# Kernel tuning notes

Measured on AMD Instinct MI355X. Metric: run time of the kernel, lower is better.

Reference implementation:

```python
import jax, jax.numpy as jnp
import numpy as np

EPS = 1e-6  # matches torch F.normalize eps used in pytorch3d lighting

def _normalize(x):
    n = jnp.linalg.norm(x, axis=-1, keepdims=True)
    return x / jnp.maximum(n, EPS)

def _interp(pix_to_face, bary, face_attrs):
    # interpolate_face_attributes: (N,H,W,K), (N,H,W,K,3), (F,3,D) -> (N,H,W,K,D)
    mask = (pix_to_face < 0)[..., None]
    idx = jnp.maximum(pix_to_face, 0)
    vals = face_attrs[idx]                      # (N,H,W,K,3,D) gather
    out = jnp.einsum('nhwkv,nhwkvd->nhwkd', bary, vals)
    return jnp.where(mask, 0.0, out)

def setup_inputs() -> dict:
    key = jax.random.key(0)
    ks = jax.random.split(key, 16)
    N, H, W, K = 8, 512, 512, 1
    V, F = 100000, 200000
    p2f = jax.random.randint(ks[0], (N, H, W, K), 0, F)
    bg = jax.random.uniform(ks[1], (N, H, W, K)) < 0.1
    pix_to_face = jnp.where(bg, -1, p2f)
    bary = jax.random.uniform(ks[2], (N, H, W, K, 3))
    bary = bary / bary.sum(-1, keepdims=True)             # valid barycentrics
    verts = jax.random.normal(ks[3], (V, 3), dtype=jnp.float32)
    verts_normals = _normalize(jax.random.normal(ks[4], (V, 3), dtype=jnp.float32))
    verts_colors = jax.random.uniform(ks[5], (V, 3), dtype=jnp.float32)
    faces = jax.random.randint(ks[6], (F, 3), 0, V)
    return {
        'pix_to_face': pix_to_face,
        'bary_coords': bary.astype(jnp.float32),
        'verts': verts,
        'verts_normals': verts_normals,
        'verts_colors': verts_colors,
        'faces': faces,
        'light_location': jax.random.normal(ks[7], (N, 3), dtype=jnp.float32) * 3.0,
        'light_ambient': jnp.full((1, 3), 0.5, jnp.float32),
        'light_diffuse': jnp.full((1, 3), 0.3, jnp.float32),
        'light_specular': jnp.full((1, 3), 0.2, jnp.float32),
        'mat_ambient': jnp.ones((1, 3), jnp.float32),
        'mat_diffuse': jnp.ones((1, 3), jnp.float32),
        'mat_specular': jnp.ones((1, 3), jnp.float32),
        'shininess': jnp.array([64.0], jnp.float32),
        'camera_pos': jax.random.normal(ks[8], (N, 3), dtype=jnp.float32) * 3.0,
        'background': jnp.ones((3,), jnp.float32),
    }

def reference(pix_to_face, bary_coords, verts, verts_normals, verts_colors, faces,
              light_location, light_ambient, light_diffuse, light_specular,
              mat_ambient, mat_diffuse, mat_specular, shininess,
              camera_pos, background):
    # ---- texture sampling (TexturesVertex) + face-attribute interpolation ----
    faces_verts = verts[faces]            # (F,3,3)
    faces_normals = verts_normals[faces]  # (F,3,3)
    faces_colors = verts_colors[faces]    # (F,3,3)
    points = _interp(pix_to_face, bary_coords, faces_verts)    # (N,H,W,K,3)
    normals = _interp(pix_to_face, bary_coords, faces_normals) # (N,H,W,K,3)
    texels = _interp(pix_to_face, bary_coords, faces_colors)   # (N,H,W,K,3)
    # ---- per-pixel Phong lighting (PointLights) ----
    loc = light_location[:, None, None, None, :]
    cam = camera_pos[:, None, None, None, :]
    n = _normalize(normals)
    to_light = _normalize(loc - points)
    cos_angle = (n * to_light).sum(-1)                         # (N,H,W,K)
    light_diff = light_diffuse * jnp.maximum(cos_angle, 0.0)[..., None]
    smask = (cos_angle > 0).astype(points.dtype)
    cos_m = cos_angle * smask
    view_dir = _normalize(cam - points)
    reflect = -to_light + 2.0 * cos_m[..., None] * n
    alpha = jnp.maximum((view_dir * reflect).sum(-1), 0.0) * smask
    alpha_safe = jnp.where(alpha > 0, alpha, 1.0)
    spec_pow = jnp.where(alpha > 0, alpha_safe ** shininess, 0.0)
    light_spec = light_specular * spec_pow[..., None]
    ambient = mat_ambient * light_ambient                       # (1,3)
    diffuse = mat_diffuse * light_diff
    specular = mat_specular * light_spec
    colors = (ambient + diffuse) * texels + specular            # (N,H,W,K,3)
    # ---- hard RGB blend ----
    is_bg = pix_to_face[..., 0] < 0                             # (N,H,W)
    rgb = jnp.where(is_bg[..., None], background, colors[..., 0, :])
    a = (~is_bg).astype(rgb.dtype)[..., None]
    return jnp.concatenate([rgb, a], axis=-1)                   # (N,H,W,4)
```

## Files before the change

kernel.cpp:

```cpp
#include <hip/hip_runtime.h>
#include <hip/hip_bf16.h>

#define EPS 1e-6f

__device__ __forceinline__ float3 ld3(const float* p, int i) {
    return make_float3(p[3*i+0], p[3*i+1], p[3*i+2]);
}
__device__ __forceinline__ float3 add3(float3 a, float3 b) {
    return make_float3(a.x+b.x, a.y+b.y, a.z+b.z);
}
__device__ __forceinline__ float3 sub3(float3 a, float3 b) {
    return make_float3(a.x-b.x, a.y-b.y, a.z-b.z);
}
__device__ __forceinline__ float3 scale3(float s, float3 a) {
    return make_float3(s*a.x, s*a.y, s*a.z);
}
__device__ __forceinline__ float dot3(float3 a, float3 b) {
    return a.x*b.x + a.y*b.y + a.z*b.z;
}
__device__ __forceinline__ float3 norm3(float3 a) {
    float n = sqrtf(dot3(a, a));
    float inv = 1.0f / fmaxf(n, EPS);
    return scale3(inv, a);
}

__global__ __launch_bounds__(256) void gather_faces_kernel(
    const float* __restrict__ verts,
    const float* __restrict__ vnorm,
    const float* __restrict__ vcol,
    const int* __restrict__ faces,
    float* __restrict__ fa,
    int F)
{
    int f = blockIdx.x * blockDim.x + threadIdx.x;
    if (f >= F) return;
    int v0 = faces[3*f+0];
    int v1 = faces[3*f+1];
    int v2 = faces[3*f+2];

    float3 p0 = ld3(verts, v0), p1 = ld3(verts, v1), p2 = ld3(verts, v2);
    float3 n0 = ld3(vnorm, v0), n1 = ld3(vnorm, v1), n2 = ld3(vnorm, v2);
    float3 c0 = ld3(vcol,  v0), c1 = ld3(vcol,  v1), c2 = ld3(vcol,  v2);

    float4* r = reinterpret_cast<float4*>(fa + 28*f);
    r[0] = make_float4(p0.x, p0.y, p0.z, p1.x);
    r[1] = make_float4(p1.y, p1.z, p2.x, p2.y);
    r[2] = make_float4(p2.z, n0.x, n0.y, n0.z);
    r[3] = make_float4(n1.x, n1.y, n1.z, n2.x);
    r[4] = make_float4(n2.y, n2.z, c0.x, c0.y);
    r[5] = make_float4(c0.z, c1.x, c1.y, c1.z);
    r[6] = make_float4(c2.x, c2.y, c2.z, 0.0f);
}

__global__ __launch_bounds__(256) void phong_kernel2(
    const int* __restrict__ p2f,
    const float* __restrict__ bary,
    const float* __restrict__ fa,
    const float* __restrict__ light_loc,
    const float* __restrict__ l_amb,
    const float* __restrict__ l_diff,
    const float* __restrict__ l_spec,
    const float* __restrict__ m_amb,
    const float* __restrict__ m_diff,
    const float* __restrict__ m_spec,
    const float* __restrict__ shin,
    const float* __restrict__ cam,
    const float* __restrict__ bg,
    float* __restrict__ out,
    int total, int hw)
{
    int idx = blockIdx.x * blockDim.x + threadIdx.x;
    if (idx >= total) return;

    int f = p2f[idx];
    float4 o;
    if (f < 0) {
        o = make_float4(bg[0], bg[1], bg[2], 0.0f);
    } else {
        float b0 = bary[3*idx+0];
        float b1 = bary[3*idx+1];
        float b2 = bary[3*idx+2];

        const float4* r = reinterpret_cast<const float4*>(fa + 28*f);
        float4 q0 = r[0], q1 = r[1], q2 = r[2], q3 = r[3],
               q4 = r[4], q5 = r[5], q6 = r[6];

        float3 p0 = make_float3(q0.x, q0.y, q0.z);
        float3 p1 = make_float3(q0.w, q1.x, q1.y);
        float3 p2 = make_float3(q1.z, q1.w, q2.x);
        float3 n0 = make_float3(q2.y, q2.z, q2.w);
        float3 n1 = make_float3(q3.x, q3.y, q3.z);
        float3 n2 = make_float3(q3.w, q4.x, q4.y);
        float3 c0 = make_float3(q4.z, q4.w, q5.x);
        float3 c1 = make_float3(q5.y, q5.z, q5.w);
        float3 c2 = make_float3(q6.x, q6.y, q6.z);

        float3 p  = add3(add3(scale3(b0, p0), scale3(b1, p1)), scale3(b2, p2));
        float3 nr = add3(add3(scale3(b0, n0), scale3(b1, n1)), scale3(b2, n2));
        float3 tx = add3(add3(scale3(b0, c0), scale3(b1, c1)), scale3(b2, c2));

        int n_b = (unsigned)idx / (unsigned)hw;
        float3 loc = ld3(light_loc, n_b);
        float3 cm  = ld3(cam, n_b);

        float3 n  = norm3(nr);
        float3 tl = norm3(sub3(loc, p));
        float cos_angle = dot3(n, tl);
        float cos_pos = fmaxf(cos_angle, 0.0f);
        float smask = (cos_angle > 0.0f) ? 1.0f : 0.0f;
        float cos_m = cos_angle * smask;

        float3 vd = norm3(sub3(cm, p));
        float3 refl = add3(scale3(-1.0f, tl), scale3(2.0f * cos_m, n));
        float alpha = fmaxf(dot3(vd, refl), 0.0f) * smask;
        float spec_pow = (alpha > 0.0f) ? powf(alpha, shin[0]) : 0.0f;

        float c0o = (m_amb[0]*l_amb[0] + m_diff[0]*l_diff[0]*cos_pos) * tx.x + m_spec[0]*l_spec[0]*spec_pow;
        float c1o = (m_amb[1]*l_amb[1] + m_diff[1]*l_diff[1]*cos_pos) * tx.y + m_spec[1]*l_spec[1]*spec_pow;
        float c2o = (m_amb[2]*l_amb[2] + m_diff[2]*l_diff[2]*cos_pos) * tx.z + m_spec[2]*l_spec[2]*spec_pow;
        o = make_float4(c0o, c1o, c2o, 1.0f);
    }
    reinterpret_cast<float4*>(out)[idx] = o;
}

__global__ __launch_bounds__(256) void phong_kernel1(
    const int* __restrict__ p2f,
    const float* __restrict__ bary,
    const float* __restrict__ verts,
    const float* __restrict__ vnorm,
    const float* __restrict__ vcol,
    const int* __restrict__ faces,
    const float* __restrict__ light_loc,
    const float* __restrict__ l_amb,
    const float* __restrict__ l_diff,
    const float* __restrict__ l_spec,
    const float* __restrict__ m_amb,
    const float* __restrict__ m_diff,
    const float* __restrict__ m_spec,
    const float* __restrict__ shin,
    const float* __restrict__ cam,
    const float* __restrict__ bg,
    float* __restrict__ out,
    int total, int hw)
{
    int idx = blockIdx.x * blockDim.x + threadIdx.x;
    if (idx >= total) return;

    int f = p2f[idx];
    float4 o;
    if (f < 0) {
        o = make_float4(bg[0], bg[1], bg[2], 0.0f);
    } else {
        float b0 = bary[3*idx+0];
        float b1 = bary[3*idx+1];
        float b2 = bary[3*idx+2];
        int v0 = faces[3*f+0];
        int v1 = faces[3*f+1];
        int v2 = faces[3*f+2];

        float3 p = add3(add3(scale3(b0, ld3(verts, v0)),
                             scale3(b1, ld3(verts, v1))),
                             scale3(b2, ld3(verts, v2)));
        float3 nr = add3(add3(scale3(b0, ld3(vnorm, v0)),
                              scale3(b1, ld3(vnorm, v1))),
                              scale3(b2, ld3(vnorm, v2)));
        float3 tx = add3(add3(scale3(b0, ld3(vcol, v0)),
                              scale3(b1, ld3(vcol, v1))),
                              scale3(b2, ld3(vcol, v2)));

        int n_b = (unsigned)idx / (unsigned)hw;
        float3 loc = ld3(light_loc, n_b);
        float3 cm  = ld3(cam, n_b);

        float3 n  = norm3(nr);
        float3 tl = norm3(sub3(loc, p));
        float cos_angle = dot3(n, tl);
        float cos_pos = fmaxf(cos_angle, 0.0f);
        float smask = (cos_angle > 0.0f) ? 1.0f : 0.0f;
        float cos_m = cos_angle * smask;

        float3 vd = norm3(sub3(cm, p));
        float3 refl = add3(scale3(-1.0f, tl), scale3(2.0f * cos_m, n));
        float alpha = fmaxf(dot3(vd, refl), 0.0f) * smask;
        float spec_pow = (alpha > 0.0f) ? powf(alpha, shin[0]) : 0.0f;

        float c0o = (m_amb[0]*l_amb[0] + m_diff[0]*l_diff[0]*cos_pos) * tx.x + m_spec[0]*l_spec[0]*spec_pow;
        float c1o = (m_amb[1]*l_amb[1] + m_diff[1]*l_diff[1]*cos_pos) * tx.y + m_spec[1]*l_spec[1]*spec_pow;
        float c2o = (m_amb[2]*l_amb[2] + m_diff[2]*l_diff[2]*cos_pos) * tx.z + m_spec[2]*l_spec[2]*spec_pow;
        o = make_float4(c0o, c1o, c2o, 1.0f);
    }
    reinterpret_cast<float4*>(out)[idx] = o;
}

extern "C" void kernel_launch(void* const* d_in, const int* in_sizes, int n_in,
                              void* d_out, int out_size, void* d_ws, size_t ws_size,
                              hipStream_t stream) {
    const int*   p2f       = (const int*)  d_in[0];
    const float* bary      = (const float*)d_in[1];
    const float* verts     = (const float*)d_in[2];
    const float* vnorm     = (const float*)d_in[3];
    const float* vcol      = (const float*)d_in[4];
    const int*   faces     = (const int*)  d_in[5];
    const float* light_loc = (const float*)d_in[6];
    const float* l_amb     = (const float*)d_in[7];
    const float* l_diff    = (const float*)d_in[8];
    const float* l_spec    = (const float*)d_in[9];
    const float* m_amb     = (const float*)d_in[10];
    const float* m_diff    = (const float*)d_in[11];
    const float* m_spec    = (const float*)d_in[12];
    const float* shin      = (const float*)d_in[13];
    const float* cam       = (const float*)d_in[14];
    const float* bg        = (const float*)d_in[15];
    float* out = (float*)d_out;

    int total   = in_sizes[0];
    int n_batch = in_sizes[6] / 3;
    int hw      = total / n_batch;
    int F       = in_sizes[5] / 3;

    int block = 256;
    size_t needed = (size_t)F * 28 * sizeof(float);

    if (ws_size >= needed) {
        float* fa = (float*)d_ws;
        int grid1 = (F + block - 1) / block;
        gather_faces_kernel<<<grid1, block, 0, stream>>>(verts, vnorm, vcol, faces, fa, F);
        int grid2 = (total + block - 1) / block;
        phong_kernel2<<<grid2, block, 0, stream>>>(
            p2f, bary, fa, light_loc,
            l_amb, l_diff, l_spec, m_amb, m_diff, m_spec, shin, cam, bg,
            out, total, hw);
    } else {
        int grid = (total + block - 1) / block;
        phong_kernel1<<<grid, block, 0, stream>>>(
            p2f, bary, verts, vnorm, vcol, faces, light_loc,
            l_amb, l_diff, l_spec, m_amb, m_diff, m_spec, shin, cam, bg,
            out, total, hw);
    }
}
```

Measured before the change: 191.0 us.

## Process two pixels per thread and pad face records to 128 bytes

Each thread in the shading kernel now handles two adjacent pixels, using vectorized int2/float2 loads for face indices and barycentrics and writing two float4 outputs. Face records are padded to a stride of 8 float4 (128 bytes) when the workspace is large enough, so each gathered record is aligned to a cache-line boundary. Background pixels are clamped to face 0 and computed branch-free, then masked, which removes divergence but does extra work on roughly a tenth of the pixels. Fewer threads each with more in-flight loads may raise register pressure and lower occupancy.

```diff
diff --git a/kernel.cpp b/kernel.cpp
--- a/kernel.cpp
+++ b/kernel.cpp
@@ -1,5 +1,4 @@
 #include <hip/hip_runtime.h>
-#include <hip/hip_bf16.h>
 
 #define EPS 1e-6f
 
@@ -23,14 +22,19 @@
     float inv = 1.0f / fmaxf(n, EPS);
     return scale3(inv, a);
 }
+
+union Rec {
+    float4 q[7];
+    float  f[28];
+};
 
 __global__ __launch_bounds__(256) void gather_faces_kernel(
     const float* __restrict__ verts,
     const float* __restrict__ vnorm,
     const float* __restrict__ vcol,
     const int* __restrict__ faces,
-    float* __restrict__ fa,
-    int F)
+    float4* __restrict__ fa,
+    int F, int stride)
 {
     int f = blockIdx.x * blockDim.x + threadIdx.x;
     if (f >= F) return;
@@ -38,24 +42,26 @@
     int v1 = faces[3*f+1];
     int v2 = faces[3*f+2];
 
-    float3 p0 = ld3(verts, v0), p1 = ld3(verts, v1), p2 = ld3(verts, v2);
-    float3 n0 = ld3(vnorm, v0), n1 = ld3(vnorm, v1), n2 = ld3(vnorm, v2);
-    float3 c0 = ld3(vcol,  v0), c1 = ld3(vcol,  v1), c2 = ld3(vcol,  v2);
-
-    float4* r = reinterpret_cast<float4*>(fa + 28*f);
-    r[0] = make_float4(p0.x, p0.y, p0.z, p1.x);
-    r[1] = make_float4(p1.y, p1.z, p2.x, p2.y);
-    r[2] = make_float4(p2.z, n0.x, n0.y, n0.z);
-    r[3] = make_float4(n1.x, n1.y, n1.z, n2.x);
-    r[4] = make_float4(n2.y, n2.z, c0.x, c0.y);
-    r[5] = make_float4(c0.z, c1.x, c1.y, c1.z);
-    r[6] = make_float4(c2.x, c2.y, c2.z, 0.0f);
+    Rec u;
+#define PUT3(base, src, vi) \
+    u.f[base+0] = src[3*vi+0]; \
+    u.f[base+1] = src[3*vi+1]; \
+    u.f[base+2] = src[3*vi+2];
+    PUT3(0,  verts, v0)  PUT3(3,  verts, v1)  PUT3(6,  verts, v2)
+    PUT3(9,  vnorm, v0)  PUT3(12, vnorm, v1)  PUT3(15, vnorm, v2)
+    PUT3(18, vcol,  v0)  PUT3(21, vcol,  v1)  PUT3(24, vcol,  v2)
+#undef PUT3
+    u.f[27] = 0.0f;
+
+    float4* r = fa + (size_t)f * stride;
+#pragma unroll
+    for (int i = 0; i < 7; ++i) r[i] = u.q[i];
 }
 
 __global__ __launch_bounds__(256) void phong_kernel2(
     const int* __restrict__ p2f,
     const float* __restrict__ bary,
-    const float* __restrict__ fa,
+    const float4* __restrict__ fa,
     const float* __restrict__ light_loc,
     const float* __restrict__ l_amb,
     const float* __restrict__ l_diff,
@@ -67,41 +73,64 @@
     const float* __restrict__ cam,
     const float* __restrict__ bg,
     float* __restrict__ out,
-    int total, int hw)
+    int total, int hw, int stride)
 {
-    int idx = blockIdx.x * blockDim.x + threadIdx.x;
-    if (idx >= total) return;
-
-    int f = p2f[idx];
-    float4 o;
-    if (f < 0) {
-        o = make_float4(bg[0], bg[1], bg[2], 0.0f);
-    } else {
-        float b0 = bary[3*idx+0];
-        float b1 = bary[3*idx+1];
-        float b2 = bary[3*idx+2];
-
-        const float4* r = reinterpret_cast<const float4*>(fa + 28*f);
-        float4 q0 = r[0], q1 = r[1], q2 = r[2], q3 = r[3],
-               q4 = r[4], q5 = r[5], q6 = r[6];
-
-        float3 p0 = make_float3(q0.x, q0.y, q0.z);
-        float3 p1 = make_float3(q0.w, q1.x, q1.y);
-        float3 p2 = make_float3(q1.z, q1.w, q2.x);
-        float3 n0 = make_float3(q2.y, q2.z, q2.w);
-        float3 n1 = make_float3(q3.x, q3.y, q3.z);
-        float3 n2 = make_float3(q3.w, q4.x, q4.y);
-        float3 c0 = make_float3(q4.z, q4.w, q5.x);
-        float3 c1 = make_float3(q5.y, q5.z, q5.w);
-        float3 c2 = make_float3(q6.x, q6.y, q6.z);
-
-        float3 p  = add3(add3(scale3(b0, p0), scale3(b1, p1)), scale3(b2, p2));
-        float3 nr = add3(add3(scale3(b0, n0), scale3(b1, n1)), scale3(b2, n2));
-        float3 tx = add3(add3(scale3(b0, c0), scale3(b1, c1)), scale3(b2, c2));
-
-        int n_b = (unsigned)idx / (unsigned)hw;
-        float3 loc = ld3(light_loc, n_b);
-        float3 cm  = ld3(cam, n_b);
+    int t = blockIdx.x * blockDim.x + threadIdx.x;
+    int i0 = 2*t;
+    if (i0 >= total) return;
+
+    int2 ff = *reinterpret_cast<const int2*>(p2f + i0);
+    float2 ba = *reinterpret_cast<const float2*>(bary + 3*i0 + 0);
+    float2 bb = *reinterpret_cast<const float2*>(bary + 3*i0 + 2);
+    float2 bc = *reinterpret_cast<const float2*>(bary + 3*i0 + 4);
+
+    int g0 = ff.x < 0 ? 0 : ff.x;
+    int g1 = ff.y < 0 ? 0 : ff.y;
+
+    const float4* r0p = fa + (size_t)g0 * stride;
+    const float4* r1p = fa + (size_t)g1 * stride;
+    Rec r0, r1;
+#pragma unroll
+    for (int i = 0; i < 7; ++i) r0.q[i] = r0p[i];
+#pragma unroll
+    for (int i = 0; i < 7; ++i) r1.q[i] = r1p[i];
+
+    int n_b = (unsigned)i0 / (unsigned)hw;
+    float3 loc = ld3(light_loc, n_b);
+    float3 cm  = ld3(cam, n_b);
+
+    float la0 = l_amb[0], la1 = l_amb[1], la2 = l_amb[2];
+    float ld0 = l_diff[0], ld1 = l_diff[1], ld2 = l_diff[2];
+    float ls0 = l_spec[0], ls1 = l_spec[1], ls2 = l_spec[2];
+    float ma0 = m_amb[0], ma1 = m_amb[1], ma2 = m_amb[2];
+    float md0 = m_diff[0], md1 = m_diff[1], md2 = m_diff[2];
+    float ms0 = m_spec[0], ms1 = m_spec[1], ms2 = m_spec[2];
+    float sh  = shin[0];
+    float bg0 = bg[0], bg1 = bg[1], bg2 = bg[2];
+
+    float4 o[2];
+    float b0s[2] = {ba.x, bb.y};
+    float b1s[2] = {ba.y, bc.x};
+    float b2s[2] = {bb.x, bc.y};
+    int fs[2] = {ff.x, ff.y};
+
+#pragma unroll
+    for (int k = 0; k < 2; ++k) {
+        const float* h = (k == 0) ? r0.f : r1.f;
+        float b0 = b0s[k], b1 = b1s[k], b2 = b2s[k];
+
+        float3 p = make_float3(
+            b0*h[0] + b1*h[3] + b2*h[6],
+            b0*h[1] + b1*h[4] + b2*h[7],
+            b0*h[2] + b1*h[5] + b2*h[8]);
+        float3 nr = make_float3(
+            b0*h[9]  + b1*h[12] + b2*h[15],
+            b0*h[10] + b1*h[13] + b2*h[16],
+            b0*h[11] + b1*h[14] + b2*h[17]);
+        float3 tx = make_float3(
+            b0*h[18] + b1*h[21] + b2*h[24],
+            b0*h[19] + b1*h[22] + b2*h[25],
+            b0*h[20] + b1*h[23] + b2*h[26]);
 
         float3 n  = norm3(nr);
         float3 tl = norm3(sub3(loc, p));
@@ -113,14 +142,20 @@
         float3 vd = norm3(sub3(cm, p));
         float3 refl = add3(scale3(-1.0f, tl), scale3(2.0f * cos_m, n));
         float alpha = fmaxf(dot3(vd, refl), 0.0f) * smask;
-        float spec_pow = (alpha > 0.0f) ? powf(alpha, shin[0]) : 0.0f;
-
-        float c0o = (m_amb[0]*l_amb[0] + m_diff[0]*l_diff[0]*cos_pos) * tx.x + m_spec[0]*l_spec[0]*spec_pow;
-        float c1o = (m_amb[1]*l_amb[1] + m_diff[1]*l_diff[1]*cos_pos) * tx.y + m_spec[1]*l_spec[1]*spec_pow;
-        float c2o = (m_amb[2]*l_amb[2] + m_diff[2]*l_diff[2]*cos_pos) * tx.z + m_spec[2]*l_spec[2]*spec_pow;
-        o = make_float4(c0o, c1o, c2o, 1.0f);
+        float spec_pow = (alpha > 0.0f) ? powf(alpha, sh) : 0.0f;
+
+        float c0o = (ma0*la0 + md0*ld0*cos_pos) * tx.x + ms0*ls0*spec_pow;
+        float c1o = (ma1*la1 + md1*ld1*cos_pos) * tx.y + ms1*ls1*spec_pow;
+        float c2o = (ma2*la2 + md2*ld2*cos_pos) * tx.z + ms2*ls2*spec_pow;
+
+        bool isbg = fs[k] < 0;
+        o[k] = isbg ? make_float4(bg0, bg1, bg2, 0.0f)
+                    : make_float4(c0o, c1o, c2o, 1.0f);
     }
-    reinterpret_cast<float4*>(out)[idx] = o;
+
+    float4* op = reinterpret_cast<float4*>(out + 4*(size_t)i0);
+    op[0] = o[0];
+    op[1] = o[1];
 }
 
 __global__ __launch_bounds__(256) void phong_kernel1(
@@ -219,17 +254,20 @@
     int F       = in_sizes[5] / 3;
 
     int block = 256;
-    size_t needed = (size_t)F * 28 * sizeof(float);
-
-    if (ws_size >= needed) {
-        float* fa = (float*)d_ws;
+    int stride = 0;
+    if (ws_size >= (size_t)F * 128) stride = 8;
+    else if (ws_size >= (size_t)F * 112) stride = 7;
+
+    if (stride != 0 && (total % 2) == 0) {
+        float4* fa = (float4*)d_ws;
         int grid1 = (F + block - 1) / block;
-        gather_faces_kernel<<<grid1, block, 0, stream>>>(verts, vnorm, vcol, faces, fa, F);
-        int grid2 = (total + block - 1) / block;
+        gather_faces_kernel<<<grid1, block, 0, stream>>>(verts, vnorm, vcol, faces, fa, F, stride);
+        int pairs = total / 2;
+        int grid2 = (pairs + block - 1) / block;
         phong_kernel2<<<grid2, block, 0, stream>>>(
             p2f, bary, fa, light_loc,
             l_amb, l_diff, l_spec, m_amb, m_diff, m_spec, shin, cam, bg,
-            out, total, hw);
+            out, total, hw, stride);
     } else {
         int grid = (total + block - 1) / block;
         phong_kernel1<<<grid, block, 0, stream>>>(
```

Measured after the change: 179.3 us. 6.1% less time.

## Pad face records to 128B and gather them cooperatively through LDS

Applied to the files above, without the earlier changes.

Face attribute records are padded from 112 to 128 bytes so each one is aligned to a cache line. In the shading kernel, each group of 8 lanes loads one face's record as eight float4s, so every global load instruction reads whole contiguous records instead of each thread fetching a strided 112-byte record. Records are staged in shared memory and each thread then reads its own. This adds LDS traffic and a barrier, and background pixels now do the gather and shading work before being masked. It also requires the total pixel count to be a multiple of 256.

```diff
diff --git a/kernel.cpp b/kernel.cpp
--- a/kernel.cpp
+++ b/kernel.cpp
@@ -1,5 +1,4 @@
 #include <hip/hip_runtime.h>
-#include <hip/hip_bf16.h>
 
 #define EPS 1e-6f
 
@@ -29,7 +28,7 @@
     const float* __restrict__ vnorm,
     const float* __restrict__ vcol,
     const int* __restrict__ faces,
-    float* __restrict__ fa,
+    float4* __restrict__ fa,
     int F)
 {
     int f = blockIdx.x * blockDim.x + threadIdx.x;
@@ -38,24 +37,27 @@
     int v1 = faces[3*f+1];
     int v2 = faces[3*f+2];
 
-    float3 p0 = ld3(verts, v0), p1 = ld3(verts, v1), p2 = ld3(verts, v2);
-    float3 n0 = ld3(vnorm, v0), n1 = ld3(vnorm, v1), n2 = ld3(vnorm, v2);
-    float3 c0 = ld3(vcol,  v0), c1 = ld3(vcol,  v1), c2 = ld3(vcol,  v2);
-
-    float4* r = reinterpret_cast<float4*>(fa + 28*f);
-    r[0] = make_float4(p0.x, p0.y, p0.z, p1.x);
-    r[1] = make_float4(p1.y, p1.z, p2.x, p2.y);
-    r[2] = make_float4(p2.z, n0.x, n0.y, n0.z);
-    r[3] = make_float4(n1.x, n1.y, n1.z, n2.x);
-    r[4] = make_float4(n2.y, n2.z, c0.x, c0.y);
-    r[5] = make_float4(c0.z, c1.x, c1.y, c1.z);
-    r[6] = make_float4(c2.x, c2.y, c2.z, 0.0f);
-}
-
-__global__ __launch_bounds__(256) void phong_kernel2(
+    union { float4 q[8]; float w[32]; } u;
+#define PUT3(base, src, vi) \
+    u.w[base+0] = src[3*vi+0]; \
+    u.w[base+1] = src[3*vi+1]; \
+    u.w[base+2] = src[3*vi+2];
+    PUT3(0,  verts, v0)  PUT3(3,  verts, v1)  PUT3(6,  verts, v2)
+    PUT3(9,  vnorm, v0)  PUT3(12, vnorm, v1)  PUT3(15, vnorm, v2)
+    PUT3(18, vcol,  v0)  PUT3(21, vcol,  v1)  PUT3(24, vcol,  v2)
+#undef PUT3
+    u.w[27] = 0.f; u.w[28] = 0.f; u.w[29] = 0.f; u.w[30] = 0.f; u.w[31] = 0.f;
+
+    float4* r = fa + (size_t)f * 8;
+#pragma unroll
+    for (int i = 0; i < 8; ++i) r[i] = u.q[i];
+}
+
+#define REC_W 36
+__global__ __launch_bounds__(256) void phong_kernel3(
     const int* __restrict__ p2f,
     const float* __restrict__ bary,
-    const float* __restrict__ fa,
+    const float4* __restrict__ fa,
     const float* __restrict__ light_loc,
     const float* __restrict__ l_amb,
     const float* __restrict__ l_diff,
@@ -69,57 +71,72 @@
     float* __restrict__ out,
     int total, int hw)
 {
-    int idx = blockIdx.x * blockDim.x + threadIdx.x;
-    if (idx >= total) return;
+    __shared__ float lds[4][64 * REC_W];
+
+    int lane = threadIdx.x & 63;
+    int wv   = threadIdx.x >> 6;
+    int idx  = blockIdx.x * 256 + wv * 64 + lane;
 
     int f = p2f[idx];
-    float4 o;
-    if (f < 0) {
-        o = make_float4(bg[0], bg[1], bg[2], 0.0f);
-    } else {
-        float b0 = bary[3*idx+0];
-        float b1 = bary[3*idx+1];
-        float b2 = bary[3*idx+2];
-
-        const float4* r = reinterpret_cast<const float4*>(fa + 28*f);
-        float4 q0 = r[0], q1 = r[1], q2 = r[2], q3 = r[3],
-               q4 = r[4], q5 = r[5], q6 = r[6];
-
-        float3 p0 = make_float3(q0.x, q0.y, q0.z);
-        float3 p1 = make_float3(q0.w, q1.x, q1.y);
-        float3 p2 = make_float3(q1.z, q1.w, q2.x);
-        float3 n0 = make_float3(q2.y, q2.z, q2.w);
-        float3 n1 = make_float3(q3.x, q3.y, q3.z);
-        float3 n2 = make_float3(q3.w, q4.x, q4.y);
-        float3 c0 = make_float3(q4.z, q4.w, q5.x);
-        float3 c1 = make_float3(q5.y, q5.z, q5.w);
-        float3 c2 = make_float3(q6.x, q6.y, q6.z);
-
-        float3 p  = add3(add3(scale3(b0, p0), scale3(b1, p1)), scale3(b2, p2));
-        float3 nr = add3(add3(scale3(b0, n0), scale3(b1, n1)), scale3(b2, n2));
-        float3 tx = add3(add3(scale3(b0, c0), scale3(b1, c1)), scale3(b2, c2));
-
-        int n_b = (unsigned)idx / (unsigned)hw;
-        float3 loc = ld3(light_loc, n_b);
-        float3 cm  = ld3(cam, n_b);
-
-        float3 n  = norm3(nr);
-        float3 tl = norm3(sub3(loc, p));
-        float cos_angle = dot3(n, tl);
-        float cos_pos = fmaxf(cos_angle, 0.0f);
-        float smask = (cos_angle > 0.0f) ? 1.0f : 0.0f;
-        float cos_m = cos_angle * smask;
-
-        float3 vd = norm3(sub3(cm, p));
-        float3 refl = add3(scale3(-1.0f, tl), scale3(2.0f * cos_m, n));
-        float alpha = fmaxf(dot3(vd, refl), 0.0f) * smask;
-        float spec_pow = (alpha > 0.0f) ? powf(alpha, shin[0]) : 0.0f;
-
-        float c0o = (m_amb[0]*l_amb[0] + m_diff[0]*l_diff[0]*cos_pos) * tx.x + m_spec[0]*l_spec[0]*spec_pow;
-        float c1o = (m_amb[1]*l_amb[1] + m_diff[1]*l_diff[1]*cos_pos) * tx.y + m_spec[1]*l_spec[1]*spec_pow;
-        float c2o = (m_amb[2]*l_amb[2] + m_diff[2]*l_diff[2]*cos_pos) * tx.z + m_spec[2]*l_spec[2]*spec_pow;
-        o = make_float4(c0o, c1o, c2o, 1.0f);
+    float b0 = bary[3*idx+0];
+    float b1 = bary[3*idx+1];
+    float b2 = bary[3*idx+2];
+    int g = f < 0 ? 0 : f;
+
+    float* myl = lds[wv];
+    int seg = lane & 7;
+    int sub = lane >> 3;
+
+#pragma unroll
+    for (int it = 0; it < 8; ++it) {
+        int p = it * 8 + sub;
+        int fp = __shfl(g, p, 64);
+        float4 v = fa[(size_t)fp * 8 + seg];
+        *reinterpret_cast<float4*>(&myl[p * REC_W + seg * 4]) = v;
     }
+    __syncthreads();
+
+    union { float4 q[7]; float w[28]; } r;
+    const float4* s4 = reinterpret_cast<const float4*>(&myl[lane * REC_W]);
+#pragma unroll
+    for (int i = 0; i < 7; ++i) r.q[i] = s4[i];
+    const float* h = r.w;
+
+    int n_b = (unsigned)idx / (unsigned)hw;
+    float3 loc = ld3(light_loc, n_b);
+    float3 cm  = ld3(cam, n_b);
+
+    float3 p = make_float3(
+        b0*h[0] + b1*h[3] + b2*h[6],
+        b0*h[1] + b1*h[4] + b2*h[7],
+        b0*h[2] + b1*h[5] + b2*h[8]);
+    float3 nr = make_float3(
+        b0*h[9]  + b1*h[12] + b2*h[15],
+        b0*h[10] + b1*h[13] + b2*h[16],
+        b0*h[11] + b1*h[14] + b2*h[17]);
+    float3 tx = make_float3(
+        b0*h[18] + b1*h[21] + b2*h[24],
+        b0*h[19] + b1*h[22] + b2*h[25],
+        b0*h[20] + b1*h[23] + b2*h[26]);
+
+    float3 n  = norm3(nr);
+    float3 tl = norm3(sub3(loc, p));
+    float cos_angle = dot3(n, tl);
+    float cos_pos = fmaxf(cos_angle, 0.0f);
+    float smask = (cos_angle > 0.0f) ? 1.0f : 0.0f;
+    float cos_m = cos_angle * smask;
+
+    float3 vd = norm3(sub3(cm, p));
+    float3 refl = add3(scale3(-1.0f, tl), scale3(2.0f * cos_m, n));
+    float alpha = fmaxf(dot3(vd, refl), 0.0f) * smask;
+    float spec_pow = (alpha > 0.0f) ? powf(alpha, shin[0]) : 0.0f;
+
+    float c0o = (m_amb[0]*l_amb[0] + m_diff[0]*l_diff[0]*cos_pos) * tx.x + m_spec[0]*l_spec[0]*spec_pow;
+    float c1o = (m_amb[1]*l_amb[1] + m_diff[1]*l_diff[1]*cos_pos) * tx.y + m_spec[1]*l_spec[1]*spec_pow;
+    float c2o = (m_amb[2]*l_amb[2] + m_diff[2]*l_diff[2]*cos_pos) * tx.z + m_spec[2]*l_spec[2]*spec_pow;
+
+    float4 o = (f < 0) ? make_float4(bg[0], bg[1], bg[2], 0.0f)
+                       : make_float4(c0o, c1o, c2o, 1.0f);
     reinterpret_cast<float4*>(out)[idx] = o;
 }
 
@@ -219,14 +236,14 @@
     int F       = in_sizes[5] / 3;
 
     int block = 256;
-    size_t needed = (size_t)F * 28 * sizeof(float);
-
-    if (ws_size >= needed) {
-        float* fa = (float*)d_ws;
+    bool ws_ok = ws_size >= (size_t)F * 128;
+
+    if (ws_ok && (total % 256) == 0) {
+        float4* fa = (float4*)d_ws;
         int grid1 = (F + block - 1) / block;
         gather_faces_kernel<<<grid1, block, 0, stream>>>(verts, vnorm, vcol, faces, fa, F);
-        int grid2 = (total + block - 1) / block;
-        phong_kernel2<<<grid2, block, 0, stream>>>(
+        int grid2 = total / 256;
+        phong_kernel3<<<grid2, block, 0, stream>>>(
             p2f, bary, fa, light_loc,
             l_amb, l_diff, l_spec, m_amb, m_diff, m_spec, shin, cam, bg,
             out, total, hw);
```

Result: faster. 171.4 us (-10.3%).
